# Kernel optimization log

Hardware: AMD Instinct MI355X
Metric: run time of the kernel (lower is better)

Reference implementation:

```python
import jax, jax.numpy as jnp
import numpy as np

NUM_USERS = 100000
NUM_ITEMS = 50000
N_NODES = NUM_USERS + NUM_ITEMS
LATENT_DIM = 64
N_LAYERS = 3
N_EDGES = 1200000
K = 0.8  # laplace-k blending: Graph = (1-k)*I + k*G


def setup_inputs() -> dict:
    key = jax.random.key(0)
    k1, k2, k3, k4, k5, k6, k7 = jax.random.split(key, 7)
    # xavier_uniform for embeddings: bound = sqrt(6/(fan_in+fan_out))
    bu = float(np.sqrt(6.0 / (NUM_USERS + LATENT_DIM)))
    bi = float(np.sqrt(6.0 / (NUM_ITEMS + LATENT_DIM)))
    user_emb = jax.random.uniform(k1, (NUM_USERS, LATENT_DIM), jnp.float32, -bu, bu)
    item_emb = jax.random.uniform(k2, (NUM_ITEMS, LATENT_DIM), jnp.float32, -bi, bi)
    edge_row = jax.random.randint(k3, (N_EDGES,), 0, N_NODES)
    edge_col = jax.random.randint(k4, (N_EDGES,), 0, N_NODES)
    # normalized-adjacency-like positive values
    edge_val = jax.random.uniform(k5, (N_EDGES,), jnp.float32) * 0.01
    users = jax.random.randint(k6, (4096,), 0, NUM_USERS)
    items = jax.random.randint(k7, (4096,), 0, NUM_ITEMS)
    return {"users": users, "items": items, "edge_row": edge_row,
            "edge_col": edge_col, "edge_val": edge_val,
            "user_emb": user_emb, "item_emb": item_emb}


def _spmm(edge_row, edge_col, edge_val, x):
    # y = G @ x via gather + segment_sum over static edge list
    msgs = edge_val[:, None] * x[edge_col]  # [E, D]
    return jax.ops.segment_sum(msgs, edge_row, num_segments=N_NODES)


def _computer(user_emb, item_emb, edge_row, edge_col, edge_val):
    all_emb = jnp.concatenate([user_emb, item_emb], axis=0)  # [N, D]
    acc = all_emb  # running sum of layer embeddings (mean taken at end)
    emb = all_emb
    for _ in range(N_LAYERS):
        # Graph = (1-K)*I + K*G, so spmm(Graph, emb) = (1-K)*emb + K*G@emb
        emb = (1.0 - K) * emb + K * _spmm(edge_row, edge_col, edge_val, emb)
        acc = acc + emb
    light_out = acc / (N_LAYERS + 1)  # mean over stacked layer embeddings
    return light_out[:NUM_USERS], light_out[NUM_USERS:]


def reference(users, items, edge_row, edge_col, edge_val, user_emb, item_emb):
    all_users, all_items = _computer(user_emb, item_emb, edge_row, edge_col, edge_val)
    u = all_users[users]  # [B, D]
    i = all_items[items]  # [B, D]
    gamma = jnp.sum(u * i, axis=1)  # [B]
    return gamma
```

## Files before the change

### kernel.cpp

```cpp
#include <hip/hip_runtime.h>
#include <hip/hip_fp16.h>
#include <stdint.h>
#include <string.h>


#define NUM_USERS 100000
#define NUM_ITEMS 50000
#define N_NODES   150000
#define DIM       64
#define N_EDGES   1200000
#define ND        (N_NODES * DIM)
#define NB        4096
#define NSAMP     (2 * NB)

#define ELL_W     24
#define NBKT      640
#define RPB       235
#define NROWS_PAD (NBKT * RPB)
#define BCAP      2176
#define SCAP      11
#define OVF_CAP   512

#define K1_THREADS     1024
#define K1_EDGE_BLOCKS 256
#define K1_ROUNDS      2
#define K1_CVT_BLOCKS  128

#define S1_ACC_BLOCKS  512
#define SPMM_BLOCKS    9375
#define ACC_BLOCKS     512
#define SP3_BLOCKS     512

__device__ __forceinline__ int h2i(__half2 h) { int r; memcpy(&r, &h, 4); return r; }
__device__ __forceinline__ __half2 i2h(int i) { __half2 h; memcpy(&h, &i, 4); return h; }

__device__ __forceinline__ float4 loadh4(const __half* p) {
    int2 v = *(const int2*)p;
    float2 a = __half22float2(i2h(v.x));
    float2 b = __half22float2(i2h(v.y));
    return make_float4(a.x, a.y, b.x, b.y);
}
__device__ __forceinline__ void storeh4(__half* p, float4 v) {
    int2 o;
    o.x = h2i(__floats2half2_rn(v.x, v.y));
    o.y = h2i(__floats2half2_rn(v.z, v.w));
    *(int2*)p = o;
}
__device__ __forceinline__ float4 f4fma(float v, float4 x, float4 a) {
    a.x += v * x.x; a.y += v * x.y; a.z += v * x.z; a.w += v * x.w;
    return a;
}

__global__ void k0_kernel(const int* __restrict__ users,
                          const int* __restrict__ items,
                          unsigned char* __restrict__ mask3,
                          unsigned char* __restrict__ mask2) {
    int i = blockIdx.x * blockDim.x + threadIdx.x;
    int n = -1;
    if (i < NB)          n = users[i];
    else if (i < NSAMP)  n = NUM_USERS + items[i - NB];
    if (n >= 0) { mask3[n] = 1; mask2[n] = 1; }
}

__global__ __launch_bounds__(K1_THREADS)
void k1_kernel(const int* __restrict__ erow,
               const int* __restrict__ ecol,
               const float* __restrict__ evalv,
               const float* __restrict__ ue,
               const float* __restrict__ ie,
               int* __restrict__ gtails,
               int2* __restrict__ barr,
               int4* __restrict__ ovf,
               int* __restrict__ ovf_cnt,
               const unsigned char* __restrict__ mask3,
               unsigned char* __restrict__ mask2,
               __half* __restrict__ xh) {
    __shared__ int2 stage[NBKT * SCAP];
    __shared__ int  scnt[NBKT];
    if (blockIdx.x < K1_EDGE_BLOCKS) {
        for (int k = threadIdx.x; k < NBKT; k += K1_THREADS) scnt[k] = 0;
        __syncthreads();
        for (int rnd = 0; rnd < K1_ROUNDS; ++rnd) {
            int base = ((rnd * K1_EDGE_BLOCKS + (int)blockIdx.x) * K1_THREADS
                        + (int)threadIdx.x) * 4;
            if (base < N_EDGES) {
                int4   r4 = *(const int4*)(erow + base);
                int4   c4 = *(const int4*)(ecol + base);
                float4 v4 = *(const float4*)(evalv + base);
                int   rr[4] = {r4.x, r4.y, r4.z, r4.w};
                int   cc[4] = {c4.x, c4.y, c4.z, c4.w};
                float vv[4] = {v4.x, v4.y, v4.z, v4.w};
                #pragma unroll
                for (int u = 0; u < 4; ++u) {
                    if (mask3[rr[u]]) mask2[cc[u]] = 1;
                    int b    = rr[u] / RPB;
                    int rloc = rr[u] - b * RPB;
                    int2 rec = make_int2(cc[u] | (rloc << 18), __float_as_int(vv[u]));
                    int s = atomicAdd(&scnt[b], 1);
                    if (s < SCAP) {
                        stage[b * SCAP + s] = rec;
                    } else {
                        atomicSub(&scnt[b], 1);
                        int gp = atomicAdd(&gtails[b], 1);
                        if (gp < BCAP) barr[(size_t)b * BCAP + gp] = rec;
                        else { int q = atomicAdd(ovf_cnt, 1);
                               if (q < OVF_CAP)
                                   ovf[q] = make_int4(rr[u], cc[u], __float_as_int(vv[u]), 0); }
                    }
                }
            }
            __syncthreads();
            for (int b = threadIdx.x; b < NBKT; b += K1_THREADS) {
                int c = scnt[b];
                if (c >= 8) {
                    int gp = atomicAdd(&gtails[b], 8);
                    if (gp + 8 <= BCAP) {
                        int2* dst = barr + (size_t)b * BCAP + gp;
                        #pragma unroll
                        for (int i = 0; i < 8; ++i) dst[i] = stage[b * SCAP + i];
                    } else {
                        for (int i = 0; i < 8; ++i) {
                            int2 rc = stage[b * SCAP + i];
                            if (gp + i < BCAP) barr[(size_t)b * BCAP + gp + i] = rc;
                            else { int q = atomicAdd(ovf_cnt, 1);
                                   if (q < OVF_CAP)
                                       ovf[q] = make_int4(b * RPB + (rc.x >> 18),
                                                          rc.x & 0x3FFFF, rc.y, 0); }
                        }
                    }
                    c -= 8;
                    for (int i = 0; i < c; ++i)
                        stage[b * SCAP + i] = stage[b * SCAP + 8 + i];
                    scnt[b] = c;
                }
            }
            __syncthreads();
        }
        for (int b = threadIdx.x; b < NBKT; b += K1_THREADS) {
            int c = scnt[b];
            if (c > 0) {
                int gp = atomicAdd(&gtails[b], c);
                for (int i = 0; i < c; ++i) {
                    int2 rc = stage[b * SCAP + i];
                    if (gp + i < BCAP) barr[(size_t)b * BCAP + gp + i] = rc;
                    else { int q = atomicAdd(ovf_cnt, 1);
                           if (q < OVF_CAP)
                               ovf[q] = make_int4(b * RPB + (rc.x >> 18),
                                                  rc.x & 0x3FFFF, rc.y, 0); }
                }
            }
        }
    } else {
        const int n4  = ND / 4;
        const int nu4 = NUM_USERS * DIM / 4;
        int i = ((int)blockIdx.x - K1_EDGE_BLOCKS) * K1_THREADS + (int)threadIdx.x;
        const int stride = K1_CVT_BLOCKS * K1_THREADS;
        int2* xh4 = (int2*)xh;
        for (; i < n4; i += stride) {
            float4 v = (i < nu4) ? ((const float4*)ue)[i]
                                 : ((const float4*)ie)[i - nu4];
            int2 o;
            o.x = h2i(__floats2half2_rn(v.x, v.y));
            o.y = h2i(__floats2half2_rn(v.z, v.w));
            xh4[i] = o;
        }
    }
}

__global__ __launch_bounds__(256)
void s1_kernel(const int* __restrict__ gtails,
               const int2* __restrict__ barr,
               const __half* __restrict__ xh,
               const float* __restrict__ ue,
               const float* __restrict__ ie,
               int* __restrict__ counts,
               int2* __restrict__ ell,
               int4* __restrict__ ovf,
               int* __restrict__ ovf_cnt,
               const unsigned char* __restrict__ mask2,
               const int* __restrict__ users,
               const int* __restrict__ items,
               float* __restrict__ acc_small,
               __half* __restrict__ emb_out) {
    __shared__ __align__(16) int2 lell[RPB * ELL_W];
    __shared__ int lcnt[RPB];
    const int wid  = threadIdx.x >> 6;
    const int lane = threadIdx.x & 63;
    const int g    = lane >> 4;
    const int t    = lane & 15;

    if (blockIdx.x < NBKT) {
        const int bkt   = blockIdx.x;
        const int rbase = bkt * RPB;
        for (int k = threadIdx.x; k < RPB; k += 256) lcnt[k] = 0;
        __syncthreads();
        int n = gtails[bkt];
        n = n < BCAP ? n : BCAP;
        for (int e = threadIdx.x; e < n; e += 256) {
            int2 rec = barr[(size_t)bkt * BCAP + e];
            int col  = rec.x & 0x3FFFF;
            int rloc = rec.x >> 18;
            int slot = atomicAdd(&lcnt[rloc], 1);
            if (slot < ELL_W)
                lell[rloc * ELL_W + slot] = make_int2(col, rec.y);
            else { int q = atomicAdd(ovf_cnt, 1);
                   if (q < OVF_CAP) ovf[q] = make_int4(rbase + rloc, col, rec.y, 0); }
        }
        __syncthreads();
        {
            int4* g4 = (int4*)(ell + (size_t)rbase * ELL_W);
            const int4* l4 = (const int4*)lell;
            for (int idx = threadIdx.x; idx < RPB * (ELL_W / 2); idx += 256) {
                int row = idx / (ELL_W / 2);
                if (rbase + row < N_NODES && mask2[rbase + row]) g4[idx] = l4[idx];
            }
            for (int k = threadIdx.x; k < RPB; k += 256)
                if (rbase + k < N_NODES && mask2[rbase + k])
                    counts[rbase + k] = lcnt[k];
        }
        int novf = *ovf_cnt;
        novf = novf < OVF_CAP ? novf : OVF_CAP;
        for (int k = 0; k < 15; ++k) {
            int rloc = wid * 4 + g + 16 * k;
            if (rloc >= RPB) break;
            int row = rbase + rloc;
            if (row >= N_NODES) continue;
            int cnt = lcnt[rloc];
            cnt = cnt < ELL_W ? cnt : ELL_W;
            const int2* ep = &lell[rloc * ELL_W];
            float4 a0 = {0,0,0,0}, a1 = {0,0,0,0}, a2 = {0,0,0,0}, a3 = {0,0,0,0};
            int j = 0;
            for (; j + 4 <= cnt; j += 4) {
                int4 cv0 = *(const int4*)(ep + j);
                int4 cv1 = *(const int4*)(ep + j + 2);
                float4 x0 = loadh4(xh + (size_t)cv0.x * DIM + t * 4);
                float4 x1 = loadh4(xh + (size_t)cv0.z * DIM + t * 4);
                float4 x2 = loadh4(xh + (size_t)cv1.x * DIM + t * 4);
                float4 x3 = loadh4(xh + (size_t)cv1.z * DIM + t * 4);
                a0 = f4fma(__int_as_float(cv0.y), x0, a0);
                a1 = f4fma(__int_as_float(cv0.w), x1, a1);
                a2 = f4fma(__int_as_float(cv1.y), x2, a2);
                a3 = f4fma(__int_as_float(cv1.w), x3, a3);
            }
            for (; j + 2 <= cnt; j += 2) {
                int4 cv = *(const int4*)(ep + j);
                float4 x0 = loadh4(xh + (size_t)cv.x * DIM + t * 4);
                float4 x1 = loadh4(xh + (size_t)cv.z * DIM + t * 4);
                a0 = f4fma(__int_as_float(cv.y), x0, a0);
                a1 = f4fma(__int_as_float(cv.w), x1, a1);
            }
            if (j < cnt) {
                int2 cv = ep[j];
                float4 xv = loadh4(xh + (size_t)cv.x * DIM + t * 4);
                a0 = f4fma(__int_as_float(cv.y), xv, a0);
            }
            for (int q = 0; q < novf; ++q) {
                int4 o = ovf[q];
                if (o.x == row) {
                    float4 xv = loadh4(xh + (size_t)o.y * DIM + t * 4);
                    a0 = f4fma(__int_as_float(o.z), xv, a0);
                }
            }
            float4 self = loadh4(xh + (size_t)row * DIM + t * 4);
            float4 r;
            r.x = 0.2f * self.x + 0.8f * ((a0.x + a1.x) + (a2.x + a3.x));
            r.y = 0.2f * self.y + 0.8f * ((a0.y + a1.y) + (a2.y + a3.y));
            r.z = 0.2f * self.z + 0.8f * ((a0.z + a1.z) + (a2.z + a3.z));
            r.w = 0.2f * self.w + 0.8f * ((a0.w + a1.w) + (a2.w + a3.w));
            storeh4(emb_out + (size_t)row * DIM + t * 4, r);
        }
    } else {
        const int s = ((int)blockIdx.x - NBKT) * 16 + wid * 4 + g;
        const int node = (s < NB) ? users[s] : (NUM_USERS + items[s - NB]);
        const float* p = (node < NUM_USERS) ? ue + (size_t)node * DIM
                                            : ie + (size_t)(node - NUM_USERS) * DIM;
        *(float4*)(acc_small + (size_t)s * DIM + t * 4) = *(const float4*)(p + t * 4);
    }
}

__global__ void spmm_kernel(const int* __restrict__ counts,
                            const int2* __restrict__ ell,
                            const __half* __restrict__ xsrc,
                            const unsigned char* __restrict__ mask,
                            const int* __restrict__ ovf_cnt,
                            const int4* __restrict__ ovf,
                            const int* __restrict__ users,
                            const int* __restrict__ items,
                            float* __restrict__ acc_small,
                            __half* __restrict__ xout) {
    const int wid  = threadIdx.x >> 6;
    const int lane = threadIdx.x & 63;
    const int g    = lane >> 4;
    const int t    = lane & 15;

    if (blockIdx.x < SPMM_BLOCKS) {
        const int row = blockIdx.x * 16 + wid * 4 + g;
        bool active = mask[row] != 0;
        int cnt = 0;
        if (active) {
            cnt = counts[row];
            cnt = cnt < ELL_W ? cnt : ELL_W;
        }
        const int2* ep = ell + (size_t)row * ELL_W;
        float4 a0 = {0,0,0,0}, a1 = {0,0,0,0}, a2 = {0,0,0,0}, a3 = {0,0,0,0};
        int j = 0;
        for (; j + 4 <= cnt; j += 4) {
            int4 cv0 = *(const int4*)(ep + j);
            int4 cv1 = *(const int4*)(ep + j + 2);
            float4 x0 = loadh4(xsrc + (size_t)cv0.x * DIM + t * 4);
            float4 x1 = loadh4(xsrc + (size_t)cv0.z * DIM + t * 4);
            float4 x2 = loadh4(xsrc + (size_t)cv1.x * DIM + t * 4);
            float4 x3 = loadh4(xsrc + (size_t)cv1.z * DIM + t * 4);
            a0 = f4fma(__int_as_float(cv0.y), x0, a0);
            a1 = f4fma(__int_as_float(cv0.w), x1, a1);
            a2 = f4fma(__int_as_float(cv1.y), x2, a2);
            a3 = f4fma(__int_as_float(cv1.w), x3, a3);
        }
        for (; j + 2 <= cnt; j += 2) {
            int4 cv = *(const int4*)(ep + j);
            float4 x0 = loadh4(xsrc + (size_t)cv.x * DIM + t * 4);
            float4 x1 = loadh4(xsrc + (size_t)cv.z * DIM + t * 4);
            a0 = f4fma(__int_as_float(cv.y), x0, a0);
            a1 = f4fma(__int_as_float(cv.w), x1, a1);
        }
        if (j < cnt) {
            int2 cv = ep[j];
            float4 xv = loadh4(xsrc + (size_t)cv.x * DIM + t * 4);
            a0 = f4fma(__int_as_float(cv.y), xv, a0);
        }
        int novf = *ovf_cnt;
        if (novf > 0) {
            novf = novf < OVF_CAP ? novf : OVF_CAP;
            for (int k = 0; k < novf; ++k) {
                int4 o = ovf[k];
                if (active && o.x == row) {
                    float4 xv = loadh4(xsrc + (size_t)o.y * DIM + t * 4);
                    a0 = f4fma(__int_as_float(o.z), xv, a0);
                }
            }
        }
        if (active) {
            float4 self = loadh4(xsrc + (size_t)row * DIM + t * 4);
            float4 r;
            r.x = 0.2f * self.x + 0.8f * ((a0.x + a1.x) + (a2.x + a3.x));
            r.y = 0.2f * self.y + 0.8f * ((a0.y + a1.y) + (a2.y + a3.y));
            r.z = 0.2f * self.z + 0.8f * ((a0.z + a1.z) + (a2.z + a3.z));
            r.w = 0.2f * self.w + 0.8f * ((a0.w + a1.w) + (a2.w + a3.w));
            storeh4(xout + (size_t)row * DIM + t * 4, r);
        }
    } else {
        const int s = (blockIdx.x - SPMM_BLOCKS) * 16 + wid * 4 + g;
        const int node = (s < NB) ? users[s] : (NUM_USERS + items[s - NB]);
        float4 v = loadh4(xsrc + (size_t)node * DIM + t * 4);
        float4* ap = (float4*)(acc_small + (size_t)s * DIM + t * 4);
        float4 a = *ap;
        a.x += v.x; a.y += v.y; a.z += v.z; a.w += v.w;
        *ap = a;
    }
}

__global__ void sp3_kernel(const int* __restrict__ counts,
                           const int2* __restrict__ ell,
                           const __half* __restrict__ emb2,
                           const int* __restrict__ ovf_cnt,
                           const int4* __restrict__ ovf,
                           const int* __restrict__ users,
                           const int* __restrict__ items,
                           float* __restrict__ acc_small) {
    const int wid  = threadIdx.x >> 6;
    const int lane = threadIdx.x & 63;
    const int g    = lane >> 4;
    const int t    = lane & 15;
    const int s = blockIdx.x * 16 + wid * 4 + g;
    if (s >= NSAMP) return;
    const int node = (s < NB) ? users[s] : (NUM_USERS + items[s - NB]);

    int cnt = counts[node];
    cnt = cnt < ELL_W ? cnt : ELL_W;
    const int2* ep = ell + (size_t)node * ELL_W;
    float4 a0 = {0,0,0,0}, a1 = {0,0,0,0}, a2 = {0,0,0,0}, a3 = {0,0,0,0};
    int j = 0;
    for (; j + 4 <= cnt; j += 4) {
        int4 cv0 = *(const int4*)(ep + j);
        int4 cv1 = *(const int4*)(ep + j + 2);
        float4 x0 = loadh4(emb2 + (size_t)cv0.x * DIM + t * 4);
        float4 x1 = loadh4(emb2 + (size_t)cv0.z * DIM + t * 4);
        float4 x2 = loadh4(emb2 + (size_t)cv1.x * DIM + t * 4);
        float4 x3 = loadh4(emb2 + (size_t)cv1.z * DIM + t * 4);
        a0 = f4fma(__int_as_float(cv0.y), x0, a0);
        a1 = f4fma(__int_as_float(cv0.w), x1, a1);
        a2 = f4fma(__int_as_float(cv1.y), x2, a2);
        a3 = f4fma(__int_as_float(cv1.w), x3, a3);
    }
    for (; j + 2 <= cnt; j += 2) {
        int4 cv = *(const int4*)(ep + j);
        float4 x0 = loadh4(emb2 + (size_t)cv.x * DIM + t * 4);
        float4 x1 = loadh4(emb2 + (size_t)cv.z * DIM + t * 4);
        a0 = f4fma(__int_as_float(cv.y), x0, a0);
        a1 = f4fma(__int_as_float(cv.w), x1, a1);
    }
    if (j < cnt) {
        int2 cv = ep[j];
        float4 xv = loadh4(emb2 + (size_t)cv.x * DIM + t * 4);
        a0 = f4fma(__int_as_float(cv.y), xv, a0);
    }
    int novf = *ovf_cnt;
    if (novf > 0) {
        novf = novf < OVF_CAP ? novf : OVF_CAP;
        for (int k = 0; k < novf; ++k) {
            int4 o = ovf[k];
            if (o.x == node) {
                float4 xv = loadh4(emb2 + (size_t)o.y * DIM + t * 4);
                a0 = f4fma(__int_as_float(o.z), xv, a0);
            }
        }
    }
    float4 self = loadh4(emb2 + (size_t)node * DIM + t * 4);
    float4* ap = (float4*)(acc_small + (size_t)s * DIM + t * 4);
    float4 a = *ap;
    a.x += 1.2f * self.x + 0.8f * ((a0.x + a1.x) + (a2.x + a3.x));
    a.y += 1.2f * self.y + 0.8f * ((a0.y + a1.y) + (a2.y + a3.y));
    a.z += 1.2f * self.z + 0.8f * ((a0.z + a1.z) + (a2.z + a3.z));
    a.w += 1.2f * self.w + 0.8f * ((a0.w + a1.w) + (a2.w + a3.w));
    *ap = a;
}

__global__ void dot_kernel(const float* __restrict__ acc_small,
                           float* __restrict__ out) {
    int w = (blockIdx.x * blockDim.x + threadIdx.x) >> 6;
    int lane = threadIdx.x & 63;
    if (w >= NB) return;
    float p = acc_small[w * DIM + lane] * acc_small[(NB + w) * DIM + lane];
    #pragma unroll
    for (int o = 32; o > 0; o >>= 1) p += __shfl_down(p, o, 64);
    if (lane == 0) out[w] = p * (1.0f / 16.0f);
}

extern "C" void kernel_launch(void* const* d_in, const int* in_sizes, int n_in,
                              void* d_out, int out_size, void* d_ws, size_t ws_size,
                              hipStream_t stream) {
    const int*   users = (const int*)  d_in[0];
    const int*   items = (const int*)  d_in[1];
    const int*   erow  = (const int*)  d_in[2];
    const int*   ecol  = (const int*)  d_in[3];
    const float* evalv = (const float*)d_in[4];
    const float* ue    = (const float*)d_in[5];
    const float* ie    = (const float*)d_in[6];
    float* out = (float*)d_out;

    __half* xh        = (__half*)d_ws;
    __half* emb_a     = xh + ND;
    __half* emb_b     = emb_a + ND;
    float*  acc_small = (float*)(emb_b + ND);
    int2*   barr      = (int2*)(acc_small + NSAMP * DIM);
    int2*   ell       = barr + (size_t)NBKT * BCAP;
    int*    counts    = (int*)(ell + (size_t)NROWS_PAD * ELL_W);
    int*    gtails    = counts + NROWS_PAD;
    int*    ovf_cnt   = gtails + NBKT;
    int4*   ovf       = (int4*)(((uintptr_t)(ovf_cnt + 1) + 15) & ~(uintptr_t)15);
    unsigned char* mask3 = (unsigned char*)(ovf + OVF_CAP);
    unsigned char* mask2 = mask3 + N_NODES;

    size_t zbytes = (size_t)((mask2 + N_NODES) - (unsigned char*)gtails);
    hipMemsetAsync(gtails, 0, zbytes, stream);

    k0_kernel<<<(NSAMP + 255) / 256, 256, 0, stream>>>(users, items, mask3, mask2);

    k1_kernel<<<K1_EDGE_BLOCKS + K1_CVT_BLOCKS, K1_THREADS, 0, stream>>>(
        erow, ecol, evalv, ue, ie, gtails, barr, ovf, ovf_cnt, mask3, mask2, xh);

    s1_kernel<<<NBKT + S1_ACC_BLOCKS, 256, 0, stream>>>(
        gtails, barr, xh, ue, ie, counts, ell, ovf, ovf_cnt, mask2,
        users, items, acc_small, emb_a);

    spmm_kernel<<<SPMM_BLOCKS + ACC_BLOCKS, 256, 0, stream>>>(
        counts, ell, emb_a, mask2, ovf_cnt, ovf,
        users, items, acc_small, emb_b);

    sp3_kernel<<<SP3_BLOCKS, 256, 0, stream>>>(
        counts, ell, emb_b, ovf_cnt, ovf, users, items, acc_small);

    dot_kernel<<<(NB * 64 + 255) / 256, 256, 0, stream>>>(acc_small, out);
}
```

Before: 223.0 us.

## Fold sample-mask kernel into k1 and move frontier expansion into s1

Removes the separate k0 launch by marking sampled nodes (mask3) in extra blocks of k1, and moves the 2-hop frontier expansion (mask2 from edges whose row is in mask3) out of the edge-bucketing loop into extra blocks of s1. Because mask2 is now built concurrently with s1, the ELL write-out no longer filters rows by mask2. It writes all rows, copying only the slots that are actually filled. This saves a launch and takes the per-edge mask3 lookup off the critical bucketing path. In exchange s1 reads the edge arrays again and writes more ELL data.

```diff
diff --git a/kernel.cpp b/kernel.cpp
--- a/kernel.cpp
+++ b/kernel.cpp
@@ -24,9 +24,13 @@
 #define K1_THREADS     1024
 #define K1_EDGE_BLOCKS 256
 #define K1_ROUNDS      2
+#define K1_MARK_BLOCKS 8
 #define K1_CVT_BLOCKS  128
 
 #define S1_ACC_BLOCKS  512
+#define S1_EXP_BLOCKS  2048
+#define S1_CPY_BLOCKS  586
+
 #define SPMM_BLOCKS    9375
 #define ACC_BLOCKS     512
 #define SP3_BLOCKS     512
@@ -51,29 +55,19 @@
     return a;
 }
 
-__global__ void k0_kernel(const int* __restrict__ users,
-                          const int* __restrict__ items,
-                          unsigned char* __restrict__ mask3,
-                          unsigned char* __restrict__ mask2) {
-    int i = blockIdx.x * blockDim.x + threadIdx.x;
-    int n = -1;
-    if (i < NB)          n = users[i];
-    else if (i < NSAMP)  n = NUM_USERS + items[i - NB];
-    if (n >= 0) { mask3[n] = 1; mask2[n] = 1; }
-}
-
 __global__ __launch_bounds__(K1_THREADS)
 void k1_kernel(const int* __restrict__ erow,
                const int* __restrict__ ecol,
                const float* __restrict__ evalv,
+               const int* __restrict__ users,
+               const int* __restrict__ items,
                const float* __restrict__ ue,
                const float* __restrict__ ie,
                int* __restrict__ gtails,
                int2* __restrict__ barr,
                int4* __restrict__ ovf,
                int* __restrict__ ovf_cnt,
-               const unsigned char* __restrict__ mask3,
-               unsigned char* __restrict__ mask2,
+               unsigned char* __restrict__ mask3,
                __half* __restrict__ xh) {
     __shared__ int2 stage[NBKT * SCAP];
     __shared__ int  scnt[NBKT];
@@ -92,7 +86,6 @@
                 float vv[4] = {v4.x, v4.y, v4.z, v4.w};
                 #pragma unroll
                 for (int u = 0; u < 4; ++u) {
-                    if (mask3[rr[u]]) mask2[cc[u]] = 1;
                     int b    = rr[u] / RPB;
                     int rloc = rr[u] - b * RPB;
                     int2 rec = make_int2(cc[u] | (rloc << 18), __float_as_int(vv[u]));
@@ -150,10 +143,15 @@
                 }
             }
         }
+    } else if (blockIdx.x < K1_EDGE_BLOCKS + K1_MARK_BLOCKS) {
+        int i = ((int)blockIdx.x - K1_EDGE_BLOCKS) * K1_THREADS + (int)threadIdx.x;
+        if (i < NB)         mask3[users[i]] = 1;
+        else if (i < NSAMP) mask3[NUM_USERS + items[i - NB]] = 1;
     } else {
         const int n4  = ND / 4;
         const int nu4 = NUM_USERS * DIM / 4;
-        int i = ((int)blockIdx.x - K1_EDGE_BLOCKS) * K1_THREADS + (int)threadIdx.x;
+        int i = ((int)blockIdx.x - K1_EDGE_BLOCKS - K1_MARK_BLOCKS) * K1_THREADS
+                + (int)threadIdx.x;
         const int stride = K1_CVT_BLOCKS * K1_THREADS;
         int2* xh4 = (int2*)xh;
         for (; i < n4; i += stride) {
@@ -168,7 +166,9 @@
 }
 
 __global__ __launch_bounds__(256)
-void s1_kernel(const int* __restrict__ gtails,
+void s1_kernel(const int* __restrict__ erow,
+               const int* __restrict__ ecol,
+               const int* __restrict__ gtails,
                const int2* __restrict__ barr,
                const __half* __restrict__ xh,
                const float* __restrict__ ue,
@@ -177,7 +177,8 @@
                int2* __restrict__ ell,
                int4* __restrict__ ovf,
                int* __restrict__ ovf_cnt,
-               const unsigned char* __restrict__ mask2,
+               const unsigned char* __restrict__ mask3,
+               unsigned char* __restrict__ mask2,
                const int* __restrict__ users,
                const int* __restrict__ items,
                float* __restrict__ acc_small,
@@ -210,13 +211,14 @@
         {
             int4* g4 = (int4*)(ell + (size_t)rbase * ELL_W);
             const int4* l4 = (const int4*)lell;
-            for (int idx = threadIdx.x; idx < RPB * (ELL_W / 2); idx += 256) {
-                int row = idx / (ELL_W / 2);
-                if (rbase + row < N_NODES && mask2[rbase + row]) g4[idx] = l4[idx];
-            }
-            for (int k = threadIdx.x; k < RPB; k += 256)
-                if (rbase + k < N_NODES && mask2[rbase + k])
-                    counts[rbase + k] = lcnt[k];
+            const int PPR = ELL_W / 2;
+            for (int idx = threadIdx.x; idx < RPB * PPR; idx += 256) {
+                int row = idx / PPR;
+                int pr  = idx - row * PPR;
+                int c = lcnt[row]; c = c < ELL_W ? c : ELL_W;
+                if (pr * 2 < c) g4[idx] = l4[idx];
+            }
+            for (int k = threadIdx.x; k < RPB; k += 256) counts[rbase + k] = lcnt[k];
         }
         int novf = *ovf_cnt;
         novf = novf < OVF_CAP ? novf : OVF_CAP;
@@ -269,12 +271,21 @@
             r.w = 0.2f * self.w + 0.8f * ((a0.w + a1.w) + (a2.w + a3.w));
             storeh4(emb_out + (size_t)row * DIM + t * 4, r);
         }
-    } else {
+    } else if (blockIdx.x < NBKT + S1_ACC_BLOCKS) {
         const int s = ((int)blockIdx.x - NBKT) * 16 + wid * 4 + g;
         const int node = (s < NB) ? users[s] : (NUM_USERS + items[s - NB]);
         const float* p = (node < NUM_USERS) ? ue + (size_t)node * DIM
                                             : ie + (size_t)(node - NUM_USERS) * DIM;
         *(float4*)(acc_small + (size_t)s * DIM + t * 4) = *(const float4*)(p + t * 4);
+    } else if (blockIdx.x < NBKT + S1_ACC_BLOCKS + S1_EXP_BLOCKS) {
+        int i = ((int)blockIdx.x - NBKT - S1_ACC_BLOCKS) * 256 + (int)threadIdx.x;
+        const int stride = S1_EXP_BLOCKS * 256;
+        for (; i < N_EDGES; i += stride)
+            if (mask3[erow[i]]) mask2[ecol[i]] = 1;
+    } else {
+        int i = ((int)blockIdx.x - NBKT - S1_ACC_BLOCKS - S1_EXP_BLOCKS) * 256
+                + (int)threadIdx.x;
+        if (i < N_NODES && mask3[i]) mask2[i] = 1;
     }
 }
 
@@ -464,14 +475,13 @@
     size_t zbytes = (size_t)((mask2 + N_NODES) - (unsigned char*)gtails);
     hipMemsetAsync(gtails, 0, zbytes, stream);
 
-    k0_kernel<<<(NSAMP + 255) / 256, 256, 0, stream>>>(users, items, mask3, mask2);
-
-    k1_kernel<<<K1_EDGE_BLOCKS + K1_CVT_BLOCKS, K1_THREADS, 0, stream>>>(
-        erow, ecol, evalv, ue, ie, gtails, barr, ovf, ovf_cnt, mask3, mask2, xh);
-
-    s1_kernel<<<NBKT + S1_ACC_BLOCKS, 256, 0, stream>>>(
-        gtails, barr, xh, ue, ie, counts, ell, ovf, ovf_cnt, mask2,
-        users, items, acc_small, emb_a);
+    k1_kernel<<<K1_EDGE_BLOCKS + K1_MARK_BLOCKS + K1_CVT_BLOCKS, K1_THREADS, 0, stream>>>(
+        erow, ecol, evalv, users, items, ue, ie,
+        gtails, barr, ovf, ovf_cnt, mask3, xh);
+
+    s1_kernel<<<NBKT + S1_ACC_BLOCKS + S1_EXP_BLOCKS + S1_CPY_BLOCKS, 256, 0, stream>>>(
+        erow, ecol, gtails, barr, xh, ue, ie, counts, ell, ovf, ovf_cnt,
+        mask3, mask2, users, items, acc_small, emb_a);
 
     spmm_kernel<<<SPMM_BLOCKS + ACC_BLOCKS, 256, 0, stream>>>(
         counts, ell, emb_a, mask2, ovf_cnt, ovf,
```

Measured after the change: 211.7 us. 5.1% less time.
